# Performance work log

Hardware: AMD Instinct MI355X
Metric: run time of the kernel (lower is better)

The kernel has to match this reference:

```python
import jax, jax.numpy as jnp
import numpy as np

LM_TEMP = 2.0      # opts.lm_temp
LAMBDA_SH = 20.0   # lambda_sh passed in ot_loss
EPS = 1e-8


def sinkhorn(M, a, b, lam, num_iter_max=1000, stop_thr=0.005):
    """Faithful port of sinkhorn_pytorch. M:[S,V], a:[S,B], b:[V,B]."""
    K = jnp.exp(-M * lam)          # [S,V]
    KM = K * M
    u0 = jnp.ones_like(a) / a.shape[0]
    v0 = jnp.zeros_like(b)

    def cond(state):
        cpt, u, v, err = state
        return (cpt < num_iter_max) & (err > stop_thr)

    def body(state):
        cpt, u, v, err = state
        u = a / (K @ (b / (u.T @ K).T))   # fused fixed-point step
        cpt = cpt + 1
        do_check = ((cpt % 20) == 1) | (cpt == num_iter_max)

        def check(uve):
            u, v, _ = uve
            v = b / (K.T @ u)
            u = a / (K @ v)
            bb = v * (K.T @ u)
            err = jnp.max(jnp.sum(jnp.abs(bb - b), axis=0))  # inf-norm over batch
            return u, v, err

        u, v, err = jax.lax.cond(do_check, check, lambda t: t, (u, v, err))
        return cpt, u, v, err

    state0 = (jnp.asarray(0, jnp.int32), u0, v0, jnp.asarray(1.0, M.dtype))
    _, u, v, _ = jax.lax.while_loop(cond, body, state0)
    return jnp.sum(u * (KM @ v), axis=0)   # [B] sinkhorn divergences


def setup_inputs() -> dict:
    key = jax.random.key(0)
    ks = jax.random.split(key, 6)
    B, H, V, NV, MAX_SLOTS = 512, 1024, 28996, 3000, 33
    inputs = jax.random.normal(ks[0], (B, 2 * H), jnp.float32)
    outputs = jax.random.normal(ks[1], (B, 512), jnp.float32)
    W_lm = jax.random.normal(ks[2], (V, H), jnp.float32) * 0.02   # lm head (no bias)
    W_lin = jax.random.normal(ks[3], (MAX_SLOTS, 512), jnp.float32) * 0.05
    b_lin = jnp.zeros((MAX_SLOTS,), jnp.float32)
    topics = jax.random.normal(ks[4], (MAX_SLOTS - 1, H), jnp.float32) * 0.01
    verbs = jax.random.randint(ks[5], (NV,), 0, V)
    return {"inputs": inputs, "outputs": outputs, "W_lm": W_lm,
            "W_lin": W_lin, "b_lin": b_lin, "topics": topics,
            "verbs": verbs, "nslots": 33}


def reference(inputs, outputs, W_lm, W_lin, b_lin, topics, verbs, nslots):
    H = W_lm.shape[1]
    # gather verb rows of the lm head once: logits[:, verbs] == x @ W_lm[verbs].T
    W_v = W_lm[verbs]                               # [NV, H]
    Wt = W_v.T                                      # [H, NV]
    o11 = jax.nn.softmax((inputs[:, :H] @ Wt) / LM_TEMP, axis=-1)
    o12 = jax.nn.softmax((inputs[:, H:] @ Wt) / LM_TEMP, axis=-1)
    o1 = (o11 + o12) * 0.5
    o1 = o1 / jnp.sum(o1, axis=1, keepdims=True)    # [B, NV] vocab marginals
    o2 = jax.nn.softmax((outputs @ W_lin.T + b_lin)[:, 1:nslots], axis=-1)  # [B, S]
    # cosine-distance cost matrix between topics and verb embeddings
    tn = topics[:nslots - 1]
    tn = tn / (jnp.linalg.norm(tn, axis=1, keepdims=True) + EPS)
    vn = W_v / (jnp.linalg.norm(W_v, axis=1, keepdims=True) + EPS)
    M = 1.0 - tn @ vn.T                             # [S, NV]
    # single chunk of ot_loss (B <= 1024): mean sinkhorn divergence
    return jnp.mean(sinkhorn(M, o2.T, o1.T, LAMBDA_SH))
```

## Files before the change

kernel.cpp:

```cpp
#include <hip/hip_runtime.h>

#define NV 3000
#define HH 1024
#define BB 512

typedef __attribute__((ext_vector_type(8))) short short8;
typedef __attribute__((ext_vector_type(4))) float floatx4;

__device__ __forceinline__ float wave_sum(float x) {
#pragma unroll
  for (int off = 32; off; off >>= 1) x += __shfl_xor(x, off, 64);
  return x;
}
__device__ __forceinline__ unsigned bf16r(float x) {
  unsigned u = __float_as_uint(x);
  u += 0x7fffu + ((u >> 16) & 1u);
  return u >> 16;
}
__device__ __forceinline__ void gload16(const void* g, void* l) {
  __builtin_amdgcn_global_load_lds(
      (const __attribute__((address_space(1))) unsigned*)g,
      (__attribute__((address_space(3))) unsigned*)l, 16, 0, 0);
}

__device__ __forceinline__ void pk_fma_acc(float2& acc, float2 a, float2 b) {
  asm("v_pk_fma_f32 %0, %1, %2, %0" : "+v"(acc) : "v"(a), "v"(b));
}
__device__ __forceinline__ float2 unpk2(unsigned d) {
  float2 r;
  r.x = __uint_as_float(d << 16);
  r.y = __uint_as_float(d & 0xffff0000u);
  return r;
}

__global__ __launch_bounds__(256) void norms_wb_kernel(
    const float* __restrict__ W_lm, const float* __restrict__ topics,
    const int* __restrict__ verbs, float* __restrict__ vninv,
    float* __restrict__ tninv, unsigned short* __restrict__ Wb) {
  int r = blockIdx.x, t = threadIdx.x;
  bool isW = r < 3072;
  int j = isW ? (r < NV ? r : NV - 1) : 0;
  const float* src = isW ? (W_lm + (size_t)verbs[j] * HH)
                         : (topics + (size_t)(r - 3072) * HH);
  float4 v = *(const float4*)(src + t * 4);
  if (isW) {
    *(uint2*)(Wb + (size_t)r * HH + t * 4) =
        make_uint2(bf16r(v.x) | (bf16r(v.y) << 16),
                   bf16r(v.z) | (bf16r(v.w) << 16));
  }
  float ss = v.x * v.x + v.y * v.y + v.z * v.z + v.w * v.w;
  ss = wave_sum(ss);
  __shared__ float sq[4];
  if ((t & 63) == 0) sq[t >> 6] = ss;
  __syncthreads();
  if (t == 0) {
    float inv = 1.0f / (sqrtf(sq[0] + sq[1] + sq[2] + sq[3]) + 1e-8f);
    if (isW) { if (r < NV) vninv[r] = inv; }
    else tninv[r - 3072] = inv;
  }
}

__global__ __launch_bounds__(256) void xb_kernel(
    const float* __restrict__ inputs, unsigned short* __restrict__ Xb) {
  int idx = blockIdx.x * 256 + threadIdx.x;
  int r = idx >> 7, c8 = (idx & 127) << 3;
  const float* src = (r < 512) ? (inputs + (size_t)r * 2048 + c8)
                               : (inputs + (size_t)(r - 512) * 2048 + 1024 + c8);
  float4 x0 = ((const float4*)src)[0];
  float4 x1 = ((const float4*)src)[1];
  uint4 o;
  o.x = bf16r(x0.x) | (bf16r(x0.y) << 16);
  o.y = bf16r(x0.z) | (bf16r(x0.w) << 16);
  o.z = bf16r(x1.x) | (bf16r(x1.y) << 16);
  o.w = bf16r(x1.z) | (bf16r(x1.w) << 16);
  *(uint4*)(Xb + (size_t)r * HH + c8) = o;
}

__global__ __launch_bounds__(256) void topt_kernel(
    const float* __restrict__ topics, const float* __restrict__ tninv,
    float* __restrict__ topT) {
  int idx = blockIdx.x * 256 + threadIdx.x;
  int k = idx >> 5, s = idx & 31;
  topT[idx] = topics[(size_t)s * HH + k] * tninv[s];
}

__global__ __launch_bounds__(64) void a_kernel(
    const float* __restrict__ outputs, const float* __restrict__ W_lin,
    const float* __restrict__ b_lin, float* __restrict__ aT) {
  int r = blockIdx.x, t = threadIdx.x;
  __shared__ float orow[512];
  __shared__ float lg[33];
  __shared__ float ms[2];
  *(float4*)(orow + t * 8)     = *(const float4*)(outputs + (size_t)r * 512 + t * 8);
  *(float4*)(orow + t * 8 + 4) = *(const float4*)(outputs + (size_t)r * 512 + t * 8 + 4);
  __syncthreads();
  if (t < 33) {
    float acc = b_lin[t];
    for (int k = 0; k < 512; ++k) acc = fmaf(orow[k], W_lin[(size_t)t * 512 + k], acc);
    lg[t] = acc;
  }
  __syncthreads();
  if (t == 0) {
    float m = lg[1];
    for (int i = 2; i < 33; ++i) m = fmaxf(m, lg[i]);
    float ssum = 0.0f;
    for (int i = 1; i < 33; ++i) ssum += __expf(lg[i] - m);
    ms[0] = m; ms[1] = ssum;
  }
  __syncthreads();
  if (t >= 1 && t < 33) aT[(size_t)r * 32 + t - 1] = __expf(lg[t] - ms[0]) / ms[1];
}

__global__ __launch_bounds__(256) void gemm_mfma(
    const unsigned short* __restrict__ Xb, const unsigned short* __restrict__ Wb,
    float* __restrict__ L) {
  __shared__ unsigned short As[128 * 32], Bs[128 * 32];
  int t = threadIdx.x;
  int wave = t >> 6, ln = t & 63;
  int bn = blockIdx.x, bm = blockIdx.y;
  int wm = (wave >> 1) * 64, wn = (wave & 1) * 64;
  const unsigned short* ga = Xb + (size_t)(bm * 128 + (t >> 2)) * HH + (t & 3) * 8;
  const unsigned short* gb = Wb + (size_t)(bn * 128 + (t >> 2)) * HH + (t & 3) * 8;
  int lq = ln >> 4, lm = ln & 15;
  floatx4 acc[4][4];
#pragma unroll
  for (int i = 0; i < 4; ++i)
#pragma unroll
    for (int j = 0; j < 4; ++j) acc[i][j] = (floatx4)0.0f;

  for (int k0 = 0; k0 < HH; k0 += 32) {
    __syncthreads();
    gload16(ga + k0, As + t * 8);
    gload16(ga + (size_t)64 * HH + k0, As + 2048 + t * 8);
    gload16(gb + k0, Bs + t * 8);
    gload16(gb + (size_t)64 * HH + k0, Bs + 2048 + t * 8);
    __syncthreads();
    short8 af[4], bfr[4];
#pragma unroll
    for (int i = 0; i < 4; ++i)
      af[i] = *(const short8*)(As + (wm + i * 16 + lm) * 32 + lq * 8);
#pragma unroll
    for (int j = 0; j < 4; ++j)
      bfr[j] = *(const short8*)(Bs + (wn + j * 16 + lm) * 32 + lq * 8);
#pragma unroll
    for (int i = 0; i < 4; ++i)
#pragma unroll
      for (int j = 0; j < 4; ++j)
        acc[i][j] = __builtin_amdgcn_mfma_f32_16x16x32_bf16(af[i], bfr[j], acc[i][j], 0, 0, 0);
  }
  int row0 = bm * 128 + wm + lq * 4;
  int col0 = bn * 128 + wn + lm;
#pragma unroll
  for (int j = 0; j < 4; ++j) {
    int col = col0 + j * 16;
    if (col < NV) {
#pragma unroll
      for (int i = 0; i < 4; ++i) {
#pragma unroll
        for (int r = 0; r < 4; ++r)
          L[(size_t)(row0 + i * 16 + r) * NV + col] = acc[i][j][r] * 0.5f;
      }
    }
  }
}

__global__ __launch_bounds__(256) void softmax_kernel(
    float* __restrict__ L1, const float* __restrict__ L2) {
  int r = blockIdx.x, t = threadIdx.x, w = t >> 6, ln = t & 63;
  float* row1 = L1 + (size_t)r * NV;
  const float* row2 = L2 + (size_t)r * NV;
  __shared__ float rd[2][4];
  float s1 = 0.0f, s2 = 0.0f;
  for (int v = t; v < NV; v += 256) { s1 += __expf(row1[v]); s2 += __expf(row2[v]); }
  s1 = wave_sum(s1); s2 = wave_sum(s2);
  if (ln == 0) { rd[0][w] = s1; rd[1][w] = s2; }
  __syncthreads();
  s1 = rd[0][0] + rd[0][1] + rd[0][2] + rd[0][3];
  s2 = rd[1][0] + rd[1][1] + rd[1][2] + rd[1][3];
  float i1 = 0.5f / s1, i2 = 0.5f / s2;
  float rs = 0.0f;
  for (int v = t; v < NV; v += 256) {
    float o = __expf(row1[v]) * i1 + __expf(row2[v]) * i2;
    row1[v] = o; rs += o;
  }
  rs = wave_sum(rs);
  __syncthreads();
  if (ln == 0) rd[0][w] = rs;
  __syncthreads();
  float rinv = 1.0f / (rd[0][0] + rd[0][1] + rd[0][2] + rd[0][3]);
  for (int v = t; v < NV; v += 256) row1[v] *= rinv;
}

__global__ __launch_bounds__(256) void mk_kernel(
    const float* __restrict__ W_lm, const int* __restrict__ verbs,
    const float* __restrict__ topT, const float* __restrict__ vninv,
    unsigned* __restrict__ Kb, float* __restrict__ KMt) {
  __shared__ float red[4][64][33];
  int t = threadIdx.x, ln = t & 63, w = t >> 6;
  int v = blockIdx.x * 64 + ln;
  int vc = v < NV ? v : NV - 1;
  int kb = __builtin_amdgcn_readfirstlane(w) << 8;
  const float* wrow = W_lm + (size_t)verbs[vc] * HH + kb;
  const float* tb = topT + (size_t)kb * 32;
  float acc[32];
#pragma unroll
  for (int s = 0; s < 32; ++s) acc[s] = 0.0f;
  for (int kk = 0; kk < 256; kk += 4) {
    float4 w4 = *(const float4*)(wrow + kk);
    const float* tr = tb + kk * 32;
    const float* pw = (const float*)&w4;
#pragma unroll
    for (int d = 0; d < 4; ++d)
#pragma unroll
      for (int s = 0; s < 32; ++s) acc[s] = fmaf(pw[d], tr[d * 32 + s], acc[s]);
  }
#pragma unroll
  for (int s = 0; s < 32; ++s) red[w][ln][s] = acc[s];
  __syncthreads();
  for (int idx = t; idx < 1024; idx += 256) {
    int l = idx >> 4, pr = idx & 15;
    int vo = blockIdx.x * 64 + l;
    if (vo < NV) {
      int s0 = pr * 2, s1 = s0 + 1;
      float vi = vninv[vo];
      float d0 = red[0][l][s0] + red[1][l][s0] + red[2][l][s0] + red[3][l][s0];
      float d1 = red[0][l][s1] + red[1][l][s1] + red[2][l][s1] + red[3][l][s1];
      float M0 = 1.0f - d0 * vi, M1 = 1.0f - d1 * vi;
      float K0 = __expf(-20.0f * M0), K1 = __expf(-20.0f * M1);
      *(float2*)(KMt + (size_t)vo * 32 + s0) = make_float2(K0 * M0, K1 * M1);
      Kb[(size_t)vo * 16 + pr] = bf16r(K0) | (bf16r(K1) << 16);
    }
  }
}

template <bool STORE_T>
__device__ __forceinline__ void kpass_ss(
    const uint4* __restrict__ Kb, const float* __restrict__ bsh0,
    const float* __restrict__ bsh1, const float2* u0, const float2* u1,
    float2* z0, float2* z1, float* vsh0, float* vsh1, int pid, int p) {
#pragma unroll 3
  for (int i = 0; i < 6; ++i) {
    int v = pid + (i << 9);
    if (i < 5 || v < NV) {
      const uint4* kq = Kb + ((size_t)v << 2) + (p << 1);
      uint4 q0 = kq[0], q1 = kq[1];
      float2 kc[8];
      kc[0] = unpk2(q0.x); kc[1] = unpk2(q0.y);
      kc[2] = unpk2(q0.z); kc[3] = unpk2(q0.w);
      kc[4] = unpk2(q1.x); kc[5] = unpk2(q1.y);
      kc[6] = unpk2(q1.z); kc[7] = unpk2(q1.w);
      float2 w0 = make_float2(0.f, 0.f), w1 = make_float2(0.f, 0.f);
#pragma unroll
      for (int j = 0; j < 8; ++j) { pk_fma_acc(w0, kc[j], u0[j]); pk_fma_acc(w1, kc[j], u1[j]); }
      float s0 = w0.x + w0.y, s1 = w1.x + w1.y;
      s0 += __shfl_xor(s0, 1, 64);
      s1 += __shfl_xor(s1, 1, 64);
      float t0 = bsh0[v] * __builtin_amdgcn_rcpf(s0);
      float t1 = bsh1[v] * __builtin_amdgcn_rcpf(s1);
      if (STORE_T && !p) { vsh0[v] = t0; vsh1[v] = t1; }
      float2 t0p = make_float2(t0, t0), t1p = make_float2(t1, t1);
#pragma unroll
      for (int j = 0; j < 8; ++j) { pk_fma_acc(z0[j], kc[j], t0p); pk_fma_acc(z1[j], kc[j], t1p); }
    }
  }
}

__device__ __forceinline__ void errpass_ss(
    const uint4* __restrict__ Kb, const float* __restrict__ bsh0,
    const float* __restrict__ bsh1, const float2* u0, const float2* u1,
    const float* vsh0, const float* vsh1, float& ep0, float& ep1,
    int pid, int p) {
#pragma unroll 3
  for (int i = 0; i < 6; ++i) {
    int v = pid + (i << 9);
    if (i < 5 || v < NV) {
      const uint4* kq = Kb + ((size_t)v << 2) + (p << 1);
      uint4 q0 = kq[0], q1 = kq[1];
      float2 kc[8];
      kc[0] = unpk2(q0.x); kc[1] = unpk2(q0.y);
      kc[2] = unpk2(q0.z); kc[3] = unpk2(q0.w);
      kc[4] = unpk2(q1.x); kc[5] = unpk2(q1.y);
      kc[6] = unpk2(q1.z); kc[7] = unpk2(q1.w);
      float2 w0 = make_float2(0.f, 0.f), w1 = make_float2(0.f, 0.f);
#pragma unroll
      for (int j = 0; j < 8; ++j) { pk_fma_acc(w0, kc[j], u0[j]); pk_fma_acc(w1, kc[j], u1[j]); }
      float s0 = w0.x + w0.y, s1 = w1.x + w1.y;
      s0 += __shfl_xor(s0, 1, 64);
      s1 += __shfl_xor(s1, 1, 64);
      if (!p) {
        ep0 += fabsf(vsh0[v] * s0 - bsh0[v]);
        ep1 += fabsf(vsh1[v] * s1 - bsh1[v]);
      }
    }
  }
}

__device__ __forceinline__ float waveRS16(float* z, int ln) {
  int cnt = 16;
#pragma unroll
  for (int d = 2; d <= 16; d <<= 1) {
    int half = cnt >> 1;
    bool hi = (ln & d) != 0;
#pragma unroll
    for (int k = 0; k < 8; ++k) {
      if (k < half) {
        float a = z[k], b = z[half + k];
        z[k] = hi ? b : a;
        z[half + k] = hi ? a : b;
      }
    }
#pragma unroll
    for (int k = 0; k < 8; ++k)
      if (k < half) z[k] += __shfl_xor(z[half + k], d, 64);
    cnt = half;
  }
  return z[0] + __shfl_xor(z[0], 32, 64);
}

__global__ __launch_bounds__(1024) void sinkhorn_kernel(
    const uint4* __restrict__ Kb, const float* __restrict__ KMt,
    const float* __restrict__ bT, const float* __restrict__ aT,
    unsigned* __restrict__ slots, float* __restrict__ outp) {
  const int t = threadIdx.x;
  const int w = t >> 6, ln = t & 63;
  const int p = t & 1, pid = t >> 1;
  const int col0 = blockIdx.x << 1;
  const float* b0r = bT + (size_t)col0 * NV;
  const float* b1r = b0r + NV;
  float* accres = (float*)(slots + 64);
  unsigned* done = slots + 65;

  __shared__ float zred[2][16][32];
  __shared__ float ush[2][32];
  __shared__ float sredA[16], sredB[16];
  __shared__ unsigned ebits;
  __shared__ float vsh0[3072], vsh1[3072];
  __shared__ float bsh0[3072], bsh1[3072];
  float* ushf = &ush[0][0];

  const int sl = ((ln & 1) << 4) | ((ln & 2) << 2) | (ln & 4) |
                 ((ln & 8) >> 2) | ((ln & 16) >> 4);

  for (int idx = t; idx < NV; idx += 1024) { bsh0[idx] = b0r[idx]; bsh1[idx] = b1r[idx]; }
  float areg = (t < 64) ? aT[(size_t)col0 * 32 + t] : 0.0f;

  float2 u0[8], u1[8];
#pragma unroll
  for (int j = 0; j < 8; ++j) {
    u0[j] = make_float2(1.0f / 32.0f, 1.0f / 32.0f);
    u1[j] = make_float2(1.0f / 32.0f, 1.0f / 32.0f);
  }
  if (t < 64) ushf[t] = 1.0f / 32.0f;
  __syncthreads();
  float err = 1.0f;
  int cpt = 0;

  while (cpt < 1000 && err > 0.005f) {
    float2 z0[8], z1[8];
#pragma unroll
    for (int j = 0; j < 8; ++j) { z0[j] = make_float2(0.0f, 0.0f); z1[j] = make_float2(0.0f, 0.0f); }
    kpass_ss<false>(Kb, bsh0, bsh1, u0, u1, z0, z1, vsh0, vsh1, pid, p);
    float r0 = waveRS16((float*)z0, ln), r1 = waveRS16((float*)z1, ln);
    __syncthreads();
    if (ln < 32) { zred[0][w][sl] = r0; zred[1][w][sl] = r1; }
    __syncthreads();
    if (t < 64) {
      int c = t >> 5, s = t & 31;
      float zz = 0.0f;
#pragma unroll
      for (int k = 0; k < 16; ++k) zz += zred[c][k][s];
      ushf[t] = areg * __builtin_amdgcn_rcpf(zz);
    }
    __syncthreads();
#pragma unroll
    for (int q = 0; q < 4; ++q) {
      *(float4*)((float*)u0 + q * 4) = *(float4*)(&ush[0][(p << 4) + q * 4]);
      *(float4*)((float*)u1 + q * 4) = *(float4*)(&ush[1][(p << 4) + q * 4]);
    }
    ++cpt;

    if (cpt % 20 == 1 || cpt == 1000) {
#pragma unroll
      for (int j = 0; j < 8; ++j) { z0[j] = make_float2(0.0f, 0.0f); z1[j] = make_float2(0.0f, 0.0f); }
      kpass_ss<true>(Kb, bsh0, bsh1, u0, u1, z0, z1, vsh0, vsh1, pid, p);
      r0 = waveRS16((float*)z0, ln); r1 = waveRS16((float*)z1, ln);
      __syncthreads();
      if (ln < 32) { zred[0][w][sl] = r0; zred[1][w][sl] = r1; }
      __syncthreads();
      if (t < 64) {
        int c = t >> 5, s = t & 31;
        float zz = 0.0f;
#pragma unroll
        for (int k = 0; k < 16; ++k) zz += zred[c][k][s];
        ushf[t] = areg * __builtin_amdgcn_rcpf(zz);
      }
      __syncthreads();
#pragma unroll
      for (int q = 0; q < 4; ++q) {
        *(float4*)((float*)u0 + q * 4) = *(float4*)(&ush[0][(p << 4) + q * 4]);
        *(float4*)((float*)u1 + q * 4) = *(float4*)(&ush[1][(p << 4) + q * 4]);
      }
      float ep0 = 0.0f, ep1 = 0.0f;
      errpass_ss(Kb, bsh0, bsh1, u0, u1, vsh0, vsh1, ep0, ep1, pid, p);
      ep0 = wave_sum(ep0); ep1 = wave_sum(ep1);
      if (ln == 0) { sredA[w] = ep0; sredB[w] = ep1; }
      __syncthreads();
      if (t == 0) {
        float e0 = 0.0f, e1 = 0.0f;
#pragma unroll
        for (int k = 0; k < 16; ++k) { e0 += sredA[k]; e1 += sredB[k]; }
        ebits = __float_as_uint(fmaxf(e0, e1));
      }
      __syncthreads();
      err = __uint_as_float(ebits);
    }
  }

  float y0[16], y1[16];
#pragma unroll
  for (int s = 0; s < 16; ++s) { y0[s] = 0.0f; y1[s] = 0.0f; }
#pragma unroll 3
  for (int i = 0; i < 6; ++i) {
    int v = pid + (i << 9);
    if (i < 5 || v < NV) {
      const float4* kp = (const float4*)(KMt + (size_t)v * 32 + (p << 4));
      float kc[16];
#pragma unroll
      for (int q = 0; q < 4; ++q) *(float4*)(kc + q * 4) = kp[q];
      float x0 = vsh0[v], x1 = vsh1[v];
#pragma unroll
      for (int s = 0; s < 16; ++s) { y0[s] = fmaf(kc[s], x0, y0[s]); y1[s] = fmaf(kc[s], x1, y1[s]); }
    }
  }
  float r0 = waveRS16(y0, ln), r1 = waveRS16(y1, ln);
  __syncthreads();
  if (ln < 32) { zred[0][w][sl] = r0; zred[1][w][sl] = r1; }
  __syncthreads();
  if (t < 64) {
    int c = t >> 5, s = t & 31;
    float ys = 0.0f;
#pragma unroll
    for (int k = 0; k < 16; ++k) ys += zred[c][k][s];
    float pp = ys * ushf[t];
#pragma unroll
    for (int off = 1; off <= 16; off <<= 1) pp += __shfl_xor(pp, off, 64);
    float other = __shfl_xor(pp, 32, 64);
    if (t == 0) {
      atomicAdd(accres, pp + other);
      __hip_atomic_fetch_add(done, 1u, __ATOMIC_RELEASE, __HIP_MEMORY_SCOPE_AGENT);
    }
  }
  if (blockIdx.x == 0 && t == 0) {
    while (__hip_atomic_load(done, __ATOMIC_ACQUIRE, __HIP_MEMORY_SCOPE_AGENT) < 256u) {
      __builtin_amdgcn_s_sleep(1);
    }
    unsigned ab = __hip_atomic_load((unsigned*)accres, __ATOMIC_RELAXED, __HIP_MEMORY_SCOPE_AGENT);
    outp[0] = __uint_as_float(ab) / 512.0f;
  }
}

extern "C" void kernel_launch(void* const* d_in, const int* in_sizes, int n_in,
                              void* d_out, int out_size, void* d_ws, size_t ws_size,
                              hipStream_t stream) {
  (void)in_sizes; (void)n_in; (void)out_size; (void)ws_size;
  const float* inputs  = (const float*)d_in[0];
  const float* outputs = (const float*)d_in[1];
  const float* W_lm    = (const float*)d_in[2];
  const float* W_lin   = (const float*)d_in[3];
  const float* b_lin   = (const float*)d_in[4];
  const float* topics  = (const float*)d_in[5];
  const int*   verbs   = (const int*)d_in[6];
  float* out = (float*)d_out;

  char* ws = (char*)d_ws;
  float*    L     = (float*)(ws);
  float*    L1    = L;
  float*    L2    = (float*)(ws + 6144000);
  float*    aT    = (float*)(ws + 12288000);
  unsigned* Kb    = (unsigned*)(ws + 12353536);
  float*    KMt   = (float*)(ws + 12545536);
  float*    topT  = (float*)(ws + 12929536);
  float*    vninv = (float*)(ws + 13060608);
  float*    tninv = (float*)(ws + 13072640);
  unsigned* slots = (unsigned*)(ws + 13072768);
  unsigned short* Xb = (unsigned short*)(ws + 13073280);
  unsigned short* Wb = (unsigned short*)(ws + 15170432);

  hipMemsetAsync((void*)slots, 0, 512, stream);

  norms_wb_kernel<<<3104, 256, 0, stream>>>(W_lm, topics, verbs, vninv, tninv, Wb);
  xb_kernel<<<512, 256, 0, stream>>>(inputs, Xb);
  topt_kernel<<<128, 256, 0, stream>>>(topics, tninv, topT);
  a_kernel<<<BB, 64, 0, stream>>>(outputs, W_lin, b_lin, aT);
  gemm_mfma<<<dim3(24, 8), 256, 0, stream>>>(Xb, Wb, L);
  softmax_kernel<<<BB, 256, 0, stream>>>(L1, L2);
  mk_kernel<<<47, 256, 0, stream>>>(W_lm, verbs, topT, vninv, Kb, KMt);
  sinkhorn_kernel<<<256, 1024, 0, stream>>>((const uint4*)Kb, KMt, L1, aT, slots, out);
}
```

Before: 385.9 us.

## Fuse prep kernels and move softmax and slot-softmax into sinkhorn prologue

Merges the norm/bf16 conversion and input bf16 conversion into one launch, merges the topic transpose into the GEMM launch as extra blocks, and folds the vocab softmax and the slot logits/softmax into the sinkhorn kernel's prologue, writing results straight into shared memory. This removes four kernel launches and the global round trip of the normalised marginals. The trade-off is more prologue work inside each sinkhorn block, which only some waves carry out, so the other waves sit idle until it finishes.

```diff
diff --git a/kernel.cpp b/kernel.cpp
--- a/kernel.cpp
+++ b/kernel.cpp
@@ -33,11 +33,29 @@
   return r;
 }
 
-__global__ __launch_bounds__(256) void norms_wb_kernel(
+__global__ __launch_bounds__(256) void prep_kernel(
     const float* __restrict__ W_lm, const float* __restrict__ topics,
     const int* __restrict__ verbs, float* __restrict__ vninv,
-    float* __restrict__ tninv, unsigned short* __restrict__ Wb) {
-  int r = blockIdx.x, t = threadIdx.x;
+    float* __restrict__ tninv, unsigned short* __restrict__ Wb,
+    const float* __restrict__ inputs, unsigned short* __restrict__ Xb) {
+  __shared__ float sq[4];
+  int rb = blockIdx.x, t = threadIdx.x;
+  if (rb >= 3104) {
+    int idx = (rb - 3104) * 256 + t;
+    int r = idx >> 7, c8 = (idx & 127) << 3;
+    const float* src = (r < 512) ? (inputs + (size_t)r * 2048 + c8)
+                                 : (inputs + (size_t)(r - 512) * 2048 + 1024 + c8);
+    float4 x0 = ((const float4*)src)[0];
+    float4 x1 = ((const float4*)src)[1];
+    uint4 o;
+    o.x = bf16r(x0.x) | (bf16r(x0.y) << 16);
+    o.y = bf16r(x0.z) | (bf16r(x0.w) << 16);
+    o.z = bf16r(x1.x) | (bf16r(x1.y) << 16);
+    o.w = bf16r(x1.z) | (bf16r(x1.w) << 16);
+    *(uint4*)(Xb + (size_t)r * HH + c8) = o;
+    return;
+  }
+  int r = rb;
   bool isW = r < 3072;
   int j = isW ? (r < NV ? r : NV - 1) : 0;
   const float* src = isW ? (W_lm + (size_t)verbs[j] * HH)
@@ -50,7 +68,6 @@
   }
   float ss = v.x * v.x + v.y * v.y + v.z * v.z + v.w * v.w;
   ss = wave_sum(ss);
-  __shared__ float sq[4];
   if ((t & 63) == 0) sq[t >> 6] = ss;
   __syncthreads();
   if (t == 0) {
@@ -60,64 +77,21 @@
   }
 }
 
-__global__ __launch_bounds__(256) void xb_kernel(
-    const float* __restrict__ inputs, unsigned short* __restrict__ Xb) {
-  int idx = blockIdx.x * 256 + threadIdx.x;
-  int r = idx >> 7, c8 = (idx & 127) << 3;
-  const float* src = (r < 512) ? (inputs + (size_t)r * 2048 + c8)
-                               : (inputs + (size_t)(r - 512) * 2048 + 1024 + c8);
-  float4 x0 = ((const float4*)src)[0];
-  float4 x1 = ((const float4*)src)[1];
-  uint4 o;
-  o.x = bf16r(x0.x) | (bf16r(x0.y) << 16);
-  o.y = bf16r(x0.z) | (bf16r(x0.w) << 16);
-  o.z = bf16r(x1.x) | (bf16r(x1.y) << 16);
-  o.w = bf16r(x1.z) | (bf16r(x1.w) << 16);
-  *(uint4*)(Xb + (size_t)r * HH + c8) = o;
-}
-
-__global__ __launch_bounds__(256) void topt_kernel(
-    const float* __restrict__ topics, const float* __restrict__ tninv,
-    float* __restrict__ topT) {
-  int idx = blockIdx.x * 256 + threadIdx.x;
-  int k = idx >> 5, s = idx & 31;
-  topT[idx] = topics[(size_t)s * HH + k] * tninv[s];
-}
-
-__global__ __launch_bounds__(64) void a_kernel(
-    const float* __restrict__ outputs, const float* __restrict__ W_lin,
-    const float* __restrict__ b_lin, float* __restrict__ aT) {
-  int r = blockIdx.x, t = threadIdx.x;
-  __shared__ float orow[512];
-  __shared__ float lg[33];
-  __shared__ float ms[2];
-  *(float4*)(orow + t * 8)     = *(const float4*)(outputs + (size_t)r * 512 + t * 8);
-  *(float4*)(orow + t * 8 + 4) = *(const float4*)(outputs + (size_t)r * 512 + t * 8 + 4);
-  __syncthreads();
-  if (t < 33) {
-    float acc = b_lin[t];
-    for (int k = 0; k < 512; ++k) acc = fmaf(orow[k], W_lin[(size_t)t * 512 + k], acc);
-    lg[t] = acc;
-  }
-  __syncthreads();
-  if (t == 0) {
-    float m = lg[1];
-    for (int i = 2; i < 33; ++i) m = fmaxf(m, lg[i]);
-    float ssum = 0.0f;
-    for (int i = 1; i < 33; ++i) ssum += __expf(lg[i] - m);
-    ms[0] = m; ms[1] = ssum;
-  }
-  __syncthreads();
-  if (t >= 1 && t < 33) aT[(size_t)r * 32 + t - 1] = __expf(lg[t] - ms[0]) / ms[1];
-}
-
-__global__ __launch_bounds__(256) void gemm_mfma(
+__global__ __launch_bounds__(256) void gt_kernel(
     const unsigned short* __restrict__ Xb, const unsigned short* __restrict__ Wb,
-    float* __restrict__ L) {
+    float* __restrict__ L, const float* __restrict__ topics,
+    const float* __restrict__ tninv, float* __restrict__ topT) {
   __shared__ unsigned short As[128 * 32], Bs[128 * 32];
   int t = threadIdx.x;
+  int b = blockIdx.x;
+  if (b >= 192) {
+    int idx = (b - 192) * 256 + t;
+    int k = idx >> 5, s = idx & 31;
+    topT[idx] = topics[(size_t)s * HH + k] * tninv[s];
+    return;
+  }
   int wave = t >> 6, ln = t & 63;
-  int bn = blockIdx.x, bm = blockIdx.y;
+  int bn = b % 24, bm = b / 24;
   int wm = (wave >> 1) * 64, wn = (wave & 1) * 64;
   const unsigned short* ga = Xb + (size_t)(bm * 128 + (t >> 2)) * HH + (t & 3) * 8;
   const unsigned short* gb = Wb + (size_t)(bn * 128 + (t >> 2)) * HH + (t & 3) * 8;
@@ -162,33 +136,6 @@
       }
     }
   }
-}
-
-__global__ __launch_bounds__(256) void softmax_kernel(
-    float* __restrict__ L1, const float* __restrict__ L2) {
-  int r = blockIdx.x, t = threadIdx.x, w = t >> 6, ln = t & 63;
-  float* row1 = L1 + (size_t)r * NV;
-  const float* row2 = L2 + (size_t)r * NV;
-  __shared__ float rd[2][4];
-  float s1 = 0.0f, s2 = 0.0f;
-  for (int v = t; v < NV; v += 256) { s1 += __expf(row1[v]); s2 += __expf(row2[v]); }
-  s1 = wave_sum(s1); s2 = wave_sum(s2);
-  if (ln == 0) { rd[0][w] = s1; rd[1][w] = s2; }
-  __syncthreads();
-  s1 = rd[0][0] + rd[0][1] + rd[0][2] + rd[0][3];
-  s2 = rd[1][0] + rd[1][1] + rd[1][2] + rd[1][3];
-  float i1 = 0.5f / s1, i2 = 0.5f / s2;
-  float rs = 0.0f;
-  for (int v = t; v < NV; v += 256) {
-    float o = __expf(row1[v]) * i1 + __expf(row2[v]) * i2;
-    row1[v] = o; rs += o;
-  }
-  rs = wave_sum(rs);
-  __syncthreads();
-  if (ln == 0) rd[0][w] = rs;
-  __syncthreads();
-  float rinv = 1.0f / (rd[0][0] + rd[0][1] + rd[0][2] + rd[0][3]);
-  for (int v = t; v < NV; v += 256) row1[v] *= rinv;
 }
 
 __global__ __launch_bounds__(256) void mk_kernel(
@@ -319,14 +266,13 @@
 
 __global__ __launch_bounds__(1024) void sinkhorn_kernel(
     const uint4* __restrict__ Kb, const float* __restrict__ KMt,
-    const float* __restrict__ bT, const float* __restrict__ aT,
+    const float* __restrict__ L, const float* __restrict__ outputs,
+    const float* __restrict__ W_lin, const float* __restrict__ b_lin,
     unsigned* __restrict__ slots, float* __restrict__ outp) {
   const int t = threadIdx.x;
   const int w = t >> 6, ln = t & 63;
   const int p = t & 1, pid = t >> 1;
   const int col0 = blockIdx.x << 1;
-  const float* b0r = bT + (size_t)col0 * NV;
-  const float* b1r = b0r + NV;
   float* accres = (float*)(slots + 64);
   unsigned* done = slots + 65;
 
@@ -336,14 +282,71 @@
   __shared__ unsigned ebits;
   __shared__ float vsh0[3072], vsh1[3072];
   __shared__ float bsh0[3072], bsh1[3072];
+  __shared__ float orow[2][512];
+  __shared__ float lgs[2][33];
+  __shared__ float ash[2][32];
+  __shared__ float rdA[2][4], rdB[2][4], rdC[2][4];
   float* ushf = &ush[0][0];
 
   const int sl = ((ln & 1) << 4) | ((ln & 2) << 2) | (ln & 4) |
                  ((ln & 8) >> 2) | ((ln & 16) >> 4);
 
-  for (int idx = t; idx < NV; idx += 1024) { bsh0[idx] = b0r[idx]; bsh1[idx] = b1r[idx]; }
-  float areg = (t < 64) ? aT[(size_t)col0 * 32 + t] : 0.0f;
-
+  const int sg = (w < 4) ? 0 : ((w >= 8 && w < 12) ? 1 : -1);
+  const int ag = (w == 4) ? 0 : ((w == 6) ? 1 : -1);
+  if (sg >= 0) {
+    int tt = (sg == 0) ? t : (t - 512);
+    const float* r1p = L + (size_t)(col0 + sg) * NV;
+    const float* r2p = L + (size_t)(512 + col0 + sg) * NV;
+    float* esh1 = sg ? bsh1 : bsh0;
+    float* esh2 = sg ? vsh1 : vsh0;
+    float s1 = 0.0f, s2 = 0.0f;
+    for (int v = tt; v < NV; v += 256) {
+      float e1 = __expf(r1p[v]), e2 = __expf(r2p[v]);
+      esh1[v] = e1; esh2[v] = e2;
+      s1 += e1; s2 += e2;
+    }
+    s1 = wave_sum(s1); s2 = wave_sum(s2);
+    if (ln == 0) { rdA[sg][w & 3] = s1; rdB[sg][w & 3] = s2; }
+  } else if (ag >= 0) {
+    const float* osrc = outputs + (size_t)(col0 + ag) * 512;
+    *(float4*)(&orow[ag][ln * 8])     = *(const float4*)(osrc + ln * 8);
+    *(float4*)(&orow[ag][ln * 8 + 4]) = *(const float4*)(osrc + ln * 8 + 4);
+    if (ln < 33) {
+      float acc = b_lin[ln];
+      for (int k = 0; k < 512; ++k)
+        acc = fmaf(orow[ag][k], W_lin[(size_t)ln * 512 + k], acc);
+      lgs[ag][ln] = acc;
+    }
+  }
+  __syncthreads();
+  if (sg >= 0) {
+    int tt = (sg == 0) ? t : (t - 512);
+    float s1 = rdA[sg][0] + rdA[sg][1] + rdA[sg][2] + rdA[sg][3];
+    float s2 = rdB[sg][0] + rdB[sg][1] + rdB[sg][2] + rdB[sg][3];
+    float i1 = 0.5f / s1, i2 = 0.5f / s2;
+    float* esh1 = sg ? bsh1 : bsh0;
+    float* esh2 = sg ? vsh1 : vsh0;
+    float rs = 0.0f;
+    for (int v = tt; v < NV; v += 256) {
+      float o = esh1[v] * i1 + esh2[v] * i2;
+      esh1[v] = o; rs += o;
+    }
+    rs = wave_sum(rs);
+    if (ln == 0) rdC[sg][w & 3] = rs;
+  } else if (ag >= 0 && ln == 0) {
+    float m = lgs[ag][1];
+    for (int i = 2; i < 33; ++i) m = fmaxf(m, lgs[ag][i]);
+    float ssum = 0.0f;
+    for (int i = 1; i < 33; ++i) ssum += __expf(lgs[ag][i] - m);
+    for (int i = 1; i < 33; ++i) ash[ag][i - 1] = __expf(lgs[ag][i] - m) / ssum;
+  }
+  __syncthreads();
+  if (sg >= 0) {
+    int tt = (sg == 0) ? t : (t - 512);
+    float rinv = 1.0f / (rdC[sg][0] + rdC[sg][1] + rdC[sg][2] + rdC[sg][3]);
+    float* esh1 = sg ? bsh1 : bsh0;
+    for (int v = tt; v < NV; v += 256) esh1[v] *= rinv;
+  }
   float2 u0[8], u1[8];
 #pragma unroll
   for (int j = 0; j < 8; ++j) {
@@ -352,6 +355,7 @@
   }
   if (t < 64) ushf[t] = 1.0f / 32.0f;
   __syncthreads();
+  const float areg = (t < 64) ? ash[t >> 5][t & 31] : 0.0f;
   float err = 1.0f;
   int cpt = 0;
 
@@ -474,9 +478,6 @@
 
   char* ws = (char*)d_ws;
   float*    L     = (float*)(ws);
-  float*    L1    = L;
-  float*    L2    = (float*)(ws + 6144000);
-  float*    aT    = (float*)(ws + 12288000);
   unsigned* Kb    = (unsigned*)(ws + 12353536);
   float*    KMt   = (float*)(ws + 12545536);
   float*    topT  = (float*)(ws + 12929536);
@@ -488,12 +489,9 @@
 
   hipMemsetAsync((void*)slots, 0, 512, stream);
 
-  norms_wb_kernel<<<3104, 256, 0, stream>>>(W_lm, topics, verbs, vninv, tninv, Wb);
-  xb_kernel<<<512, 256, 0, stream>>>(inputs, Xb);
-  topt_kernel<<<128, 256, 0, stream>>>(topics, tninv, topT);
-  a_kernel<<<BB, 64, 0, stream>>>(outputs, W_lin, b_lin, aT);
-  gemm_mfma<<<dim3(24, 8), 256, 0, stream>>>(Xb, Wb, L);
-  softmax_kernel<<<BB, 256, 0, stream>>>(L1, L2);
+  prep_kernel<<<3616, 256, 0, stream>>>(W_lm, topics, verbs, vninv, tninv, Wb, inputs, Xb);
+  gt_kernel<<<320, 256, 0, stream>>>(Xb, Wb, L, topics, tninv, topT);
   mk_kernel<<<47, 256, 0, stream>>>(W_lm, verbs, topT, vninv, Kb, KMt);
-  sinkhorn_kernel<<<256, 1024, 0, stream>>>((const uint4*)Kb, KMt, L1, aT, slots, out);
-}
+  sinkhorn_kernel<<<256, 1024, 0, stream>>>((const uint4*)Kb, KMt, L, outputs,
+                                            W_lin, b_lin, slots, out);
+}
```

Result: faster. 370.9 us (-3.9%).
